# Kernel optimization log

Measured on AMD Instinct MI355X. Metric: run time of the kernel, lower is better.

Reference implementation:

```python
import jax, jax.numpy as jnp
import numpy as np

NUM_EMBEDDINGS = 1024
EMBEDDING_DIM = 64
COMMITMENT_COST = 0.25
N_TOKENS = 262144


def setup_inputs() -> dict:
    key = jax.random.key(0)
    k1, k2 = jax.random.split(key)
    z = jax.random.normal(k1, (N_TOKENS, EMBEDDING_DIM), dtype=jnp.float32)
    # torch init: uniform_(-1/num_embeddings, 1/num_embeddings)
    lim = 1.0 / NUM_EMBEDDINGS
    weight = jax.random.uniform(k2, (NUM_EMBEDDINGS, EMBEDDING_DIM),
                                dtype=jnp.float32, minval=-lim, maxval=lim)
    return {"z": z, "weight": weight}


def reference(z, weight):
    flat_z = z.reshape(-1, EMBEDDING_DIM)                      # (N, D)
    # squared L2 distances to each code: (N, K)
    distances = (jnp.sum(flat_z ** 2, axis=1, keepdims=True)
                 + jnp.sum(weight ** 2, axis=1)
                 - 2.0 * flat_z @ weight.T)
    indices = jnp.argmin(distances, axis=1)                    # (N,)
    z_q = weight[indices]                                      # (N, D)
    e_latent_loss = jnp.mean((jax.lax.stop_gradient(z_q) - flat_z) ** 2)
    q_latent_loss = jnp.mean((z_q - jax.lax.stop_gradient(flat_z)) ** 2)
    loss = q_latent_loss + COMMITMENT_COST * e_latent_loss
    # straight-through estimator
    z_q_st = flat_z + jax.lax.stop_gradient(z_q - flat_z)
    z_q_st = z_q_st.reshape(z.shape)
    return (z_q_st, loss, indices)
```

## Files before the change

kernel.cpp:

```cpp
#include <hip/hip_runtime.h>
#include <stdint.h>

#define N_TOK 262144
#define DIM 64
#define K_CODES 1024
#define OUT_LOSS_OFF (N_TOK * DIM)
#define OUT_IDX_OFF (N_TOK * DIM + 1)

#define MARGIN 4e-4f

typedef _Float16 half8 __attribute__((ext_vector_type(8)));
typedef float f32x4 __attribute__((ext_vector_type(4)));
typedef unsigned int uint32x4 __attribute__((ext_vector_type(4)));

#define SM_WF 0
#define SM_SW2 131072
#define SM_SZ2 135168
#define SM_M1 136192
#define SM_M2 137216
#define SM_M3 138240
#define SM_I1 139264
#define SM_I2 140288
#define SM_IDX 141312
#define SM_FBC 142336
#define SM_FBL 142340
#define SM_RED 143368
#define SM_FBK 143496
#define SM_BYTES 143504

__device__ __forceinline__ float np_sumsq64_stream(const float4* p) {
#pragma clang fp contract(off)
  float r[8];
  {
    float4 a = p[0], b = p[1];
    r[0] = a.x * a.x;
    r[1] = a.y * a.y;
    r[2] = a.z * a.z;
    r[3] = a.w * a.w;
    r[4] = b.x * b.x;
    r[5] = b.y * b.y;
    r[6] = b.z * b.z;
    r[7] = b.w * b.w;
  }
#pragma unroll
  for (int i = 1; i < 8; ++i) {
    float4 a = p[2 * i], b = p[2 * i + 1];
    r[0] += a.x * a.x;
    r[1] += a.y * a.y;
    r[2] += a.z * a.z;
    r[3] += a.w * a.w;
    r[4] += b.x * b.x;
    r[5] += b.y * b.y;
    r[6] += b.z * b.z;
    r[7] += b.w * b.w;
  }
  return ((r[0] + r[1]) + (r[2] + r[3])) + ((r[4] + r[5]) + (r[6] + r[7]));
}

__device__ __forceinline__ float exact_dist(const float* __restrict__ z,
                                            long long t, int c,
                                            const float* __restrict__ w,
                                            float s_z2v, float w2) {
  const float4* zp = (const float4*)(z + (size_t)t * DIM);
  const float4* wp = (const float4*)(w + (size_t)c * DIM);
  float a = 0.f;
#pragma unroll
  for (int i = 0; i < 16; ++i) {
    float4 zv = zp[i];
    float4 pv = wp[i];
    a = __builtin_fmaf(zv.x + zv.x, pv.x, a);
    a = __builtin_fmaf(zv.y + zv.y, pv.y, a);
    a = __builtin_fmaf(zv.z + zv.z, pv.z, a);
    a = __builtin_fmaf(zv.w + zv.w, pv.w, a);
  }
  return (s_z2v + w2) - a;
}

__device__ __forceinline__ void ins3(float d, int c, float& m1, int& i1,
                                     float& m2, int& i2, float& m3) {
  bool b1 = d < m1, b2 = d < m2;
  float u1 = fmaxf(m1, d);
  m1 = fminf(m1, d);
  i2 = b1 ? i1 : (b2 ? c : i2);
  i1 = b1 ? c : i1;
  float u2 = fmaxf(m2, u1);
  m2 = fminf(m2, u1);
  m3 = fminf(m3, u2);
}

__device__ __forceinline__ void make_afrag(float4 a, float4 b, half8& hi,
                                           half8& lo) {
  float v[8] = {a.x, a.y, a.z, a.w, b.x, b.y, b.z, b.w};
  uint32x4 uh, ul;
#pragma unroll
  for (int j = 0; j < 4; ++j) {
    float x0 = v[2 * j] + v[2 * j];
    float x1 = v[2 * j + 1] + v[2 * j + 1];
    _Float16 h0 = (_Float16)x0, h1 = (_Float16)x1;
    float r0 = (x0 - (float)h0) * 4096.f;
    float r1 = (x1 - (float)h1) * 4096.f;
    _Float16 l0 = (_Float16)r0, l1 = (_Float16)r1;
    uh[j] = (unsigned)__builtin_bit_cast(unsigned short, h0) |
            ((unsigned)__builtin_bit_cast(unsigned short, h1) << 16);
    ul[j] = (unsigned)__builtin_bit_cast(unsigned short, l0) |
            ((unsigned)__builtin_bit_cast(unsigned short, l1) << 16);
  }
  hi = __builtin_bit_cast(half8, uh);
  lo = __builtin_bit_cast(half8, ul);
}

__global__ __attribute__((amdgpu_flat_work_group_size(1024, 1024),
                          amdgpu_waves_per_eu(4, 4))) void vq_main_k(
    const float* __restrict__ z, const float* __restrict__ w,
    float* __restrict__ out, double* __restrict__ loss_acc) {
#pragma clang fp contract(off)
  __shared__ __align__(16) char smem[SM_BYTES];
  char* wf = smem + SM_WF;
  float* sw2 = (float*)(smem + SM_SW2);
  float* sz2 = (float*)(smem + SM_SZ2);
  float* sm1 = (float*)(smem + SM_M1);
  float* sm2 = (float*)(smem + SM_M2);
  float* sm3 = (float*)(smem + SM_M3);
  int* si1 = (int*)(smem + SM_I1);
  int* si2 = (int*)(smem + SM_I2);
  int* sidx = (int*)(smem + SM_IDX);
  int* fbc = (int*)(smem + SM_FBC);
  int* fbl = (int*)(smem + SM_FBL);
  double* red = (double*)(smem + SM_RED);
  unsigned long long* fbk = (unsigned long long*)(smem + SM_FBK);

  const int tid = (int)threadIdx.x;
  const int lane = tid & 63;
  const int wid = tid >> 6;

  if (tid == 0) *fbc = 0;

  {
    const int c = tid;
    const float4* wp = (const float4*)(w + (size_t)c * DIM);
    float r[8];
#pragma unroll
    for (int ch = 0; ch < 8; ++ch) {
      float4 a = wp[2 * ch], b = wp[2 * ch + 1];
      float x[8] = {a.x, a.y, a.z, a.w, b.x, b.y, b.z, b.w};
      if (ch == 0) {
#pragma unroll
        for (int j = 0; j < 8; ++j) r[j] = x[j] * x[j];
      } else {
#pragma unroll
        for (int j = 0; j < 8; ++j) r[j] += x[j] * x[j];
      }
      uint32x4 pk;
#pragma unroll
      for (int j = 0; j < 4; ++j) {
        _Float16 h0 = (_Float16)(x[2 * j] * 1024.f);
        _Float16 h1 = (_Float16)(x[2 * j + 1] * 1024.f);
        pk[j] = (unsigned)__builtin_bit_cast(unsigned short, h0) |
                ((unsigned)__builtin_bit_cast(unsigned short, h1) << 16);
      }
      *(uint32x4*)(wf + c * 128 + ((ch ^ (c & 7)) << 4)) = pk;
    }
    sw2[c] = ((r[0] + r[1]) + (r[2] + r[3])) + ((r[4] + r[5]) + (r[6] + r[7]));
  }
  if (tid < 256) {
    long long gt = (long long)blockIdx.x * 256 + tid;
    sz2[tid] = np_sumsq64_stream((const float4*)(z + (size_t)gt * DIM));
  }
  __syncthreads();

  {
    const int wtok = wid * 16;
    const int g = lane >> 4;
    const int c15 = lane & 15;
    const int swz = c15 & 7;
    half8 ah0, al0, ah1, al1;
    {
      long long gA = ((long long)blockIdx.x * 256 + wtok + c15) * DIM;
      const float* zr = z + gA + g * 8;
      make_afrag(*(const float4*)(zr), *(const float4*)(zr + 4), ah0, al0);
      make_afrag(*(const float4*)(zr + 32), *(const float4*)(zr + 36), ah1,
                 al1);
    }

    float m1[4], m2[4], m3[4];
    int i1[4], i2[4];
#pragma unroll
    for (int r = 0; r < 4; ++r) {
      m1[r] = m2[r] = m3[r] = 3.4e38f;
      i1[r] = i2[r] = 0;
    }

    const float C1N = -1.f / 1024.f;
    const float C2N = -1.f / (1024.f * 4096.f);

#pragma unroll 4
    for (int ct = 0; ct < 64; ++ct) {
      const int cc = (ct << 4) | c15;
      float w2c = sw2[cc];
      const char* wrow = wf + cc * 128;
      half8 b0 = __builtin_bit_cast(
          half8, *(const uint32x4*)(wrow + ((g ^ swz) << 4)));
      half8 b1 = __builtin_bit_cast(
          half8, *(const uint32x4*)(wrow + (((4 + g) ^ swz) << 4)));
      float vm = w2c * -1024.f;
      f32x4 acch = {vm, vm, vm, vm};
      f32x4 accl = {0.f, 0.f, 0.f, 0.f};
      acch = __builtin_amdgcn_mfma_f32_16x16x32_f16(ah0, b0, acch, 0, 0, 0);
      accl = __builtin_amdgcn_mfma_f32_16x16x32_f16(al0, b0, accl, 0, 0, 0);
      acch = __builtin_amdgcn_mfma_f32_16x16x32_f16(ah1, b1, acch, 0, 0, 0);
      accl = __builtin_amdgcn_mfma_f32_16x16x32_f16(al1, b1, accl, 0, 0, 0);
#pragma unroll
      for (int r = 0; r < 4; ++r) {
        float t = acch[r] * C1N;
        float d = __builtin_fmaf(accl[r], C2N, t);
        ins3(d, cc, m1[r], i1[r], m2[r], i2[r], m3[r]);
      }
    }

#pragma unroll
    for (int s = 1; s <= 8; s <<= 1) {
#pragma unroll
      for (int r = 0; r < 4; ++r) {
        float om1 = __shfl_xor(m1[r], s, 64);
        float om2 = __shfl_xor(m2[r], s, 64);
        float om3 = __shfl_xor(m3[r], s, 64);
        int oi1 = __shfl_xor(i1[r], s, 64);
        int oi2 = __shfl_xor(i2[r], s, 64);
        ins3(om1, oi1, m1[r], i1[r], m2[r], i2[r], m3[r]);
        ins3(om2, oi2, m1[r], i1[r], m2[r], i2[r], m3[r]);
        m3[r] = fminf(m3[r], om3);
      }
    }
    if (c15 == 0) {
#pragma unroll
      for (int r = 0; r < 4; ++r) {
        int tk = wtok + g * 4 + r;
        sm1[tk] = m1[r];
        sm2[tk] = m2[r];
        sm3[tk] = m3[r];
        si1[tk] = i1[r];
        si2[tk] = i2[r];
      }
    }
  }
  __syncthreads();

  if (tid < 256) {
    const int tok = tid;
    float v1 = sm1[tok], v2 = sm2[tok], v3 = sm3[tok];
    float thr = v1 + MARGIN;
    int idx = si1[tok];
    if (v2 <= thr) {
      if (v3 <= thr) {
        int p = atomicAdd(fbc, 1);
        fbl[p] = tok;
        idx = -1;
      } else {
        long long gt = (long long)blockIdx.x * 256 + tok;
        float sz2v = sz2[tok];
        int ca = si1[tok], cb = si2[tok];
        if (cb < ca) { int t = ca; ca = cb; cb = t; }
        float bd = exact_dist(z, gt, ca, w, sz2v, sw2[ca]);
        idx = ca;
        float d2 = exact_dist(z, gt, cb, w, sz2v, sw2[cb]);
        if (d2 < bd) { bd = d2; idx = cb; }
      }
    }
    if (idx >= 0) sidx[tok] = idx;
  }
  __syncthreads();

  {
    int nfb = *fbc;
    for (int f = 0; f < nfb; ++f) {
      int tok = fbl[f];
      if (tid == 0) *fbk = ~0ull;
      __syncthreads();
      long long gt = (long long)blockIdx.x * 256 + tok;
      float d = exact_dist(z, gt, tid, w, sz2[tok], sw2[tid]);
      unsigned long long key =
          ((unsigned long long)__builtin_bit_cast(unsigned int, d) << 32) |
          (unsigned)tid;
#pragma unroll
      for (int off = 32; off > 0; off >>= 1) {
        unsigned long long o = __shfl_down(key, off, 64);
        key = (o < key) ? o : key;
      }
      if (lane == 0) atomicMin(fbk, key);
      __syncthreads();
      if (tid == 0) sidx[tok] = (int)((*fbk) & 0xffffffffu);
    }
  }
  __syncthreads();

  {
    const int tok = tid >> 2, q = tid & 3;
    const long long gt = (long long)blockIdx.x * 256 + tok;
    const int idx = sidx[tok];
    const float4* zp = (const float4*)(z + (size_t)gt * DIM) + q * 4;
    const float4* wp = (const float4*)(w + (size_t)idx * DIM) + q * 4;
    float4* op = (float4*)(out + (size_t)gt * DIM) + q * 4;
    double ls = 0.0;
#pragma unroll
    for (int i = 0; i < 4; ++i) {
      float4 wv = wp[i];
      float4 zv = zp[i];
      op[i] = wv;
      double d0 = (double)wv.x - (double)zv.x;
      double d1 = (double)wv.y - (double)zv.y;
      double d2 = (double)wv.z - (double)zv.z;
      double d3 = (double)wv.w - (double)zv.w;
      ls = __builtin_fma(d0, d0, ls);
      ls = __builtin_fma(d1, d1, ls);
      ls = __builtin_fma(d2, d2, ls);
      ls = __builtin_fma(d3, d3, ls);
    }
    if (q == 0) out[OUT_IDX_OFF + gt] = (float)idx;
#pragma unroll
    for (int off = 32; off > 0; off >>= 1) ls += __shfl_down(ls, off, 64);
    if (lane == 0) red[wid] = ls;
    __syncthreads();
    if (tid == 0) {
      double s = 0.0;
#pragma unroll
      for (int i = 0; i < 16; ++i) s += red[i];
      atomicAdd(loss_acc, s);
    }
  }
}

__global__ void vq_final_k(const double* __restrict__ loss_acc,
                           float* __restrict__ out) {
  out[OUT_LOSS_OFF] =
      (float)(1.25 * (*loss_acc) * (1.0 / (double)((size_t)N_TOK * DIM)));
}

extern "C" void kernel_launch(void* const* d_in, const int* in_sizes, int n_in,
                              void* d_out, int out_size, void* d_ws,
                              size_t ws_size, hipStream_t stream) {
  const float* z = (const float*)d_in[0];
  const float* w = (const float*)d_in[1];
  float* out = (float*)d_out;
  double* loss_acc = (double*)d_ws;

  hipMemsetAsync(d_ws, 0, 8, stream);
  vq_main_k<<<N_TOK / 256, 1024, 0, stream>>>(z, w, out, loss_acc);
  vq_final_k<<<1, 1, 0, stream>>>(loss_acc, out);
}
```

Measured before the change: 423.9 us.

## Replace hi/lo fp16 split with two-pass max-threshold candidate lists per wave

Drops the low-order fp16 MFMA pass and instead runs two fp16-only passes over the codebook. The first finds the per-token max score, the second records every code within a fixed threshold into a per-wave shared-memory list, which is then resolved with exact fp32 distances. Block-wide barriers and the serial block-level fallback loop are replaced by wave-local processing. This halves MFMA work per pass but repeats the codebook sweep. It also risks list overflow and slow per-lane scans of the full codebook, and correctness now depends on the fixed threshold bounding the fp16 error.

Result: faster. 366.9 us (-13.5%).

```diff
diff --git a/kernel.cpp b/kernel.cpp
--- a/kernel.cpp
+++ b/kernel.cpp
@@ -7,7 +7,8 @@
 #define OUT_LOSS_OFF (N_TOK * DIM)
 #define OUT_IDX_OFF (N_TOK * DIM + 1)
 
-#define MARGIN 4e-4f
+#define THRA 0.666f
+#define WCAP 256
 
 typedef _Float16 half8 __attribute__((ext_vector_type(8)));
 typedef float f32x4 __attribute__((ext_vector_type(4)));
@@ -16,17 +17,10 @@
 #define SM_WF 0
 #define SM_SW2 131072
 #define SM_SZ2 135168
-#define SM_M1 136192
-#define SM_M2 137216
-#define SM_M3 138240
-#define SM_I1 139264
-#define SM_I2 140288
-#define SM_IDX 141312
-#define SM_FBC 142336
-#define SM_FBL 142340
-#define SM_RED 143368
-#define SM_FBK 143496
-#define SM_BYTES 143504
+#define SM_WL 136192
+#define SM_WC 152576
+#define SM_RED 152640
+#define SM_BYTES 152768
 
 __device__ __forceinline__ float np_sumsq64_stream(const float4* p) {
 #pragma clang fp contract(off)
@@ -76,37 +70,17 @@
   return (s_z2v + w2) - a;
 }
 
-__device__ __forceinline__ void ins3(float d, int c, float& m1, int& i1,
-                                     float& m2, int& i2, float& m3) {
-  bool b1 = d < m1, b2 = d < m2;
-  float u1 = fmaxf(m1, d);
-  m1 = fminf(m1, d);
-  i2 = b1 ? i1 : (b2 ? c : i2);
-  i1 = b1 ? c : i1;
-  float u2 = fmaxf(m2, u1);
-  m2 = fminf(m2, u1);
-  m3 = fminf(m3, u2);
-}
-
-__device__ __forceinline__ void make_afrag(float4 a, float4 b, half8& hi,
-                                           half8& lo) {
+__device__ __forceinline__ void make_afrag_hi(float4 a, float4 b, half8& hi) {
   float v[8] = {a.x, a.y, a.z, a.w, b.x, b.y, b.z, b.w};
-  uint32x4 uh, ul;
+  uint32x4 uh;
 #pragma unroll
   for (int j = 0; j < 4; ++j) {
-    float x0 = v[2 * j] + v[2 * j];
-    float x1 = v[2 * j + 1] + v[2 * j + 1];
-    _Float16 h0 = (_Float16)x0, h1 = (_Float16)x1;
-    float r0 = (x0 - (float)h0) * 4096.f;
-    float r1 = (x1 - (float)h1) * 4096.f;
-    _Float16 l0 = (_Float16)r0, l1 = (_Float16)r1;
+    _Float16 h0 = (_Float16)(v[2 * j] + v[2 * j]);
+    _Float16 h1 = (_Float16)(v[2 * j + 1] + v[2 * j + 1]);
     uh[j] = (unsigned)__builtin_bit_cast(unsigned short, h0) |
             ((unsigned)__builtin_bit_cast(unsigned short, h1) << 16);
-    ul[j] = (unsigned)__builtin_bit_cast(unsigned short, l0) |
-            ((unsigned)__builtin_bit_cast(unsigned short, l1) << 16);
   }
   hi = __builtin_bit_cast(half8, uh);
-  lo = __builtin_bit_cast(half8, ul);
 }
 
 __global__ __attribute__((amdgpu_flat_work_group_size(1024, 1024),
@@ -118,22 +92,15 @@
   char* wf = smem + SM_WF;
   float* sw2 = (float*)(smem + SM_SW2);
   float* sz2 = (float*)(smem + SM_SZ2);
-  float* sm1 = (float*)(smem + SM_M1);
-  float* sm2 = (float*)(smem + SM_M2);
-  float* sm3 = (float*)(smem + SM_M3);
-  int* si1 = (int*)(smem + SM_I1);
-  int* si2 = (int*)(smem + SM_I2);
-  int* sidx = (int*)(smem + SM_IDX);
-  int* fbc = (int*)(smem + SM_FBC);
-  int* fbl = (int*)(smem + SM_FBL);
   double* red = (double*)(smem + SM_RED);
-  unsigned long long* fbk = (unsigned long long*)(smem + SM_FBK);
 
   const int tid = (int)threadIdx.x;
   const int lane = tid & 63;
   const int wid = tid >> 6;
 
-  if (tid == 0) *fbc = 0;
+  unsigned* wl = (unsigned*)(smem + SM_WL) + wid * WCAP;
+  int* wc = (int*)(smem + SM_WC) + wid;
+  if (lane == 0) *wc = 0;
 
   {
     const int c = tid;
@@ -168,135 +135,134 @@
   }
   __syncthreads();
 
+  const int wtok = wid * 16;
+  const int g = lane >> 4;
+  const int c15 = lane & 15;
+  const int swz = c15 & 7;
+  half8 ah0, ah1;
   {
-    const int wtok = wid * 16;
-    const int g = lane >> 4;
-    const int c15 = lane & 15;
-    const int swz = c15 & 7;
-    half8 ah0, al0, ah1, al1;
-    {
-      long long gA = ((long long)blockIdx.x * 256 + wtok + c15) * DIM;
-      const float* zr = z + gA + g * 8;
-      make_afrag(*(const float4*)(zr), *(const float4*)(zr + 4), ah0, al0);
-      make_afrag(*(const float4*)(zr + 32), *(const float4*)(zr + 36), ah1,
-                 al1);
-    }
-
-    float m1[4], m2[4], m3[4];
-    int i1[4], i2[4];
-#pragma unroll
-    for (int r = 0; r < 4; ++r) {
-      m1[r] = m2[r] = m3[r] = 3.4e38f;
-      i1[r] = i2[r] = 0;
-    }
-
-    const float C1N = -1.f / 1024.f;
-    const float C2N = -1.f / (1024.f * 4096.f);
-
+    long long gA = ((long long)blockIdx.x * 256 + wtok + c15) * DIM;
+    const float* zr = z + gA + g * 8;
+    make_afrag_hi(*(const float4*)(zr), *(const float4*)(zr + 4), ah0);
+    make_afrag_hi(*(const float4*)(zr + 32), *(const float4*)(zr + 36), ah1);
+  }
+  const char* b0base = wf + c15 * 128 + ((g ^ swz) << 4);
+  const char* b1base = wf + c15 * 128 + (((4 + g) ^ swz) << 4);
+
+  float M1[4];
+#pragma unroll
+  for (int r = 0; r < 4; ++r) M1[r] = -3.4e38f;
 #pragma unroll 4
-    for (int ct = 0; ct < 64; ++ct) {
-      const int cc = (ct << 4) | c15;
-      float w2c = sw2[cc];
-      const char* wrow = wf + cc * 128;
-      half8 b0 = __builtin_bit_cast(
-          half8, *(const uint32x4*)(wrow + ((g ^ swz) << 4)));
-      half8 b1 = __builtin_bit_cast(
-          half8, *(const uint32x4*)(wrow + (((4 + g) ^ swz) << 4)));
-      float vm = w2c * -1024.f;
-      f32x4 acch = {vm, vm, vm, vm};
-      f32x4 accl = {0.f, 0.f, 0.f, 0.f};
-      acch = __builtin_amdgcn_mfma_f32_16x16x32_f16(ah0, b0, acch, 0, 0, 0);
-      accl = __builtin_amdgcn_mfma_f32_16x16x32_f16(al0, b0, accl, 0, 0, 0);
-      acch = __builtin_amdgcn_mfma_f32_16x16x32_f16(ah1, b1, acch, 0, 0, 0);
-      accl = __builtin_amdgcn_mfma_f32_16x16x32_f16(al1, b1, accl, 0, 0, 0);
-#pragma unroll
-      for (int r = 0; r < 4; ++r) {
-        float t = acch[r] * C1N;
-        float d = __builtin_fmaf(accl[r], C2N, t);
-        ins3(d, cc, m1[r], i1[r], m2[r], i2[r], m3[r]);
-      }
-    }
-
-#pragma unroll
-    for (int s = 1; s <= 8; s <<= 1) {
-#pragma unroll
-      for (int r = 0; r < 4; ++r) {
-        float om1 = __shfl_xor(m1[r], s, 64);
-        float om2 = __shfl_xor(m2[r], s, 64);
-        float om3 = __shfl_xor(m3[r], s, 64);
-        int oi1 = __shfl_xor(i1[r], s, 64);
-        int oi2 = __shfl_xor(i2[r], s, 64);
-        ins3(om1, oi1, m1[r], i1[r], m2[r], i2[r], m3[r]);
-        ins3(om2, oi2, m1[r], i1[r], m2[r], i2[r], m3[r]);
-        m3[r] = fminf(m3[r], om3);
-      }
-    }
-    if (c15 == 0) {
-#pragma unroll
-      for (int r = 0; r < 4; ++r) {
-        int tk = wtok + g * 4 + r;
-        sm1[tk] = m1[r];
-        sm2[tk] = m2[r];
-        sm3[tk] = m3[r];
-        si1[tk] = i1[r];
-        si2[tk] = i2[r];
-      }
-    }
-  }
-  __syncthreads();
-
-  if (tid < 256) {
-    const int tok = tid;
-    float v1 = sm1[tok], v2 = sm2[tok], v3 = sm3[tok];
-    float thr = v1 + MARGIN;
-    int idx = si1[tok];
-    if (v2 <= thr) {
-      if (v3 <= thr) {
-        int p = atomicAdd(fbc, 1);
-        fbl[p] = tok;
-        idx = -1;
-      } else {
-        long long gt = (long long)blockIdx.x * 256 + tok;
-        float sz2v = sz2[tok];
-        int ca = si1[tok], cb = si2[tok];
-        if (cb < ca) { int t = ca; ca = cb; cb = t; }
-        float bd = exact_dist(z, gt, ca, w, sz2v, sw2[ca]);
-        idx = ca;
-        float d2 = exact_dist(z, gt, cb, w, sz2v, sw2[cb]);
-        if (d2 < bd) { bd = d2; idx = cb; }
-      }
-    }
-    if (idx >= 0) sidx[tok] = idx;
-  }
-  __syncthreads();
+  for (int ct = 0; ct < 64; ++ct) {
+    float w2c = sw2[(ct << 4) | c15];
+    half8 b0 =
+        __builtin_bit_cast(half8, *(const uint32x4*)(b0base + ct * 2048));
+    half8 b1 =
+        __builtin_bit_cast(half8, *(const uint32x4*)(b1base + ct * 2048));
+    float vm = w2c * -1024.f;
+    f32x4 acch = {vm, vm, vm, vm};
+    acch = __builtin_amdgcn_mfma_f32_16x16x32_f16(ah0, b0, acch, 0, 0, 0);
+    acch = __builtin_amdgcn_mfma_f32_16x16x32_f16(ah1, b1, acch, 0, 0, 0);
+#pragma unroll
+    for (int r = 0; r < 4; ++r) M1[r] = fmaxf(M1[r], acch[r]);
+  }
+#pragma unroll
+  for (int s = 1; s <= 8; s <<= 1) {
+#pragma unroll
+    for (int r = 0; r < 4; ++r)
+      M1[r] = fmaxf(M1[r], __shfl_xor(M1[r], s, 64));
+  }
+  float thr[4];
+#pragma unroll
+  for (int r = 0; r < 4; ++r) thr[r] = M1[r] - THRA;
+
+  const int tb = g * 4;
+#pragma unroll 4
+  for (int ct = 0; ct < 64; ++ct) {
+    float w2c = sw2[(ct << 4) | c15];
+    half8 b0 =
+        __builtin_bit_cast(half8, *(const uint32x4*)(b0base + ct * 2048));
+    half8 b1 =
+        __builtin_bit_cast(half8, *(const uint32x4*)(b1base + ct * 2048));
+    float vm = w2c * -1024.f;
+    f32x4 acch = {vm, vm, vm, vm};
+    acch = __builtin_amdgcn_mfma_f32_16x16x32_f16(ah0, b0, acch, 0, 0, 0);
+    acch = __builtin_amdgcn_mfma_f32_16x16x32_f16(ah1, b1, acch, 0, 0, 0);
+    const int cc = (ct << 4) | c15;
+    bool h0 = acch[0] >= thr[0];
+    bool h1 = acch[1] >= thr[1];
+    bool h2 = acch[2] >= thr[2];
+    bool h3 = acch[3] >= thr[3];
+    if (h0 | h1 | h2 | h3) {
+      if (h0) {
+        int p = atomicAdd(wc, 1);
+        if (p < WCAP) wl[p] = (unsigned)(((tb + 0) << 10) | cc);
+      }
+      if (h1) {
+        int p = atomicAdd(wc, 1);
+        if (p < WCAP) wl[p] = (unsigned)(((tb + 1) << 10) | cc);
+      }
+      if (h2) {
+        int p = atomicAdd(wc, 1);
+        if (p < WCAP) wl[p] = (unsigned)(((tb + 2) << 10) | cc);
+      }
+      if (h3) {
+        int p = atomicAdd(wc, 1);
+        if (p < WCAP) wl[p] = (unsigned)(((tb + 3) << 10) | cc);
+      }
+    }
+  }
+
+  asm volatile("s_waitcnt lgkmcnt(0)" ::: "memory");
+  int n = *wc;
+
+  int idxw = 0;
+  if (lane < 16) {
+    int cnt = 0, code = 0;
+    for (int e = 0; e < n && e < WCAP; ++e) {
+      unsigned u = wl[e];
+      if ((int)(u >> 10) == lane) {
+        cnt++;
+        code = (int)(u & 1023u);
+      }
+    }
+    if (n > WCAP) {
+      long long gt = (long long)blockIdx.x * 256 + wtok + lane;
+      float sz2v = sz2[wtok + lane];
+      float bd = 3.4e38f;
+      code = 0;
+      for (int c = 0; c < K_CODES; ++c) {
+        float d = exact_dist(z, gt, c, w, sz2v, sw2[c]);
+        if (d < bd) {
+          bd = d;
+          code = c;
+        }
+      }
+    } else if (cnt >= 2) {
+      long long gt = (long long)blockIdx.x * 256 + wtok + lane;
+      float sz2v = sz2[wtok + lane];
+      float bd = 3.4e38f;
+      int bi = K_CODES;
+      for (int e = 0; e < n; ++e) {
+        unsigned u = wl[e];
+        if ((int)(u >> 10) == lane) {
+          int c = (int)(u & 1023u);
+          float d = exact_dist(z, gt, c, w, sz2v, sw2[c]);
+          if (d < bd || (d == bd && c < bi)) {
+            bd = d;
+            bi = c;
+          }
+        }
+      }
+      code = bi;
+    }
+    idxw = code;
+  }
+  const int idx = __shfl(idxw, lane >> 2, 64);
 
   {
-    int nfb = *fbc;
-    for (int f = 0; f < nfb; ++f) {
-      int tok = fbl[f];
-      if (tid == 0) *fbk = ~0ull;
-      __syncthreads();
-      long long gt = (long long)blockIdx.x * 256 + tok;
-      float d = exact_dist(z, gt, tid, w, sz2[tok], sw2[tid]);
-      unsigned long long key =
-          ((unsigned long long)__builtin_bit_cast(unsigned int, d) << 32) |
-          (unsigned)tid;
-#pragma unroll
-      for (int off = 32; off > 0; off >>= 1) {
-        unsigned long long o = __shfl_down(key, off, 64);
-        key = (o < key) ? o : key;
-      }
-      if (lane == 0) atomicMin(fbk, key);
-      __syncthreads();
-      if (tid == 0) sidx[tok] = (int)((*fbk) & 0xffffffffu);
-    }
-  }
-  __syncthreads();
-
-  {
-    const int tok = tid >> 2, q = tid & 3;
+    const int tok = wtok + (lane >> 2), q = lane & 3;
     const long long gt = (long long)blockIdx.x * 256 + tok;
-    const int idx = sidx[tok];
     const float4* zp = (const float4*)(z + (size_t)gt * DIM) + q * 4;
     const float4* wp = (const float4*)(w + (size_t)idx * DIM) + q * 4;
     float4* op = (float4*)(out + (size_t)gt * DIM) + q * 4;
@@ -319,13 +285,13 @@
 #pragma unroll
     for (int off = 32; off > 0; off >>= 1) ls += __shfl_down(ls, off, 64);
     if (lane == 0) red[wid] = ls;
-    __syncthreads();
-    if (tid == 0) {
-      double s = 0.0;
-#pragma unroll
-      for (int i = 0; i < 16; ++i) s += red[i];
-      atomicAdd(loss_acc, s);
-    }
+  }
+  __syncthreads();
+  if (tid == 0) {
+    double s = 0.0;
+#pragma unroll
+    for (int i = 0; i < 16; ++i) s += red[i];
+    atomicAdd(loss_acc, s);
   }
 }
 
```
